# Kernel tuning notes

Hardware: AMD Instinct MI355X
Metric: run time of the kernel (lower is better)

The kernel has to match this reference:

```python
import jax, jax.numpy as jnp
import numpy as np

B, C, M, K, V, D, H, A, L, HF = 2, 128, 4, 4, 64, 1024, 16, 64, 4, 2048
E = M + K
EPS = 1e-5
THETA = 10000.0


def _rmsnorm(x, w):
    return x * jax.lax.rsqrt(jnp.mean(x * x, -1, keepdims=True) + EPS) * w


def _l2norm(x):
    n = jnp.sqrt(jnp.sum(x * x, -1, keepdims=True))
    return x / jnp.maximum(n, EPS)


def _rope(x, cos, sin):
    x1, x2 = jnp.split(x, 2, axis=-1)
    return jnp.concatenate([x1 * cos + x2 * sin, -x1 * sin + x2 * cos], -1)


def _forward(x_input, dec_w1, dec_w2, pos_emb, Wqkv, Wo, Wup, Wdown, attn_norm_w, ffn_norm_w, doc):
    b = x_input.shape[0]
    c = x_input.shape[1] // M
    # decoder_w1 then 'b (c m) (k v) -> b c k (m v)', decoder_w2, pos emb
    x = jnp.einsum('bsd,od->bso', x_input, dec_w1)
    x = x.reshape(b, c, M, K, V).transpose(0, 1, 3, 2, 4).reshape(b, c, K, M * V)
    x = jnp.einsum('bcku,du->bckd', x, dec_w2) + pos_emb
    # decoder_include_original_token: prepend original m tokens per block
    x = jnp.concatenate([x_input.reshape(b, c, M, D), x], axis=2).reshape(b, c * E, D)
    s = c * E
    # mask_mod (decoder_global_original_attn): (causal & kv%e<k & same_doc) | same_block
    idx = jnp.arange(s)
    blk = idx // E
    docs = doc[:, blk]  # [b, s]
    doc_m = docs[:, :, None] == docs[:, None, :]
    causal = blk[:, None] >= blk[None, :]
    kv_ok = (idx % E) < K
    same = blk[:, None] == blk[None, :]
    mask = (causal[None] & kv_ok[None, None, :] & doc_m) | same[None]  # [b, s, s]
    # rotary tables (applied post head-split, dim A)
    inv_freq = (1.0 / THETA) ** (jnp.arange(0, A, 2) / A)
    freqs = jnp.arange(s)[:, None] * inv_freq[None, :]
    cos, sin = jnp.cos(freqs), jnp.sin(freqs)  # [s, A/2]
    scale = 1.0 / jnp.sqrt(jnp.float32(A))
    neg = jnp.float32(-1e30)

    def heads(t):
        return t.reshape(b, s, H, A).transpose(0, 2, 1, 3)

    for li in range(L):
        xn = _rmsnorm(x, attn_norm_w[li])
        qkv = jnp.einsum('bsd,od->bso', xn, Wqkv[li])
        q, k, v = jnp.split(qkv, 3, axis=-1)
        q, k, v = heads(q), heads(k), heads(v)
        q, k = _l2norm(q), _l2norm(k)  # qk_norm
        q, k = _rope(q, cos, sin), _rope(k, cos, sin)
        scores = jnp.einsum('bhqa,bhka->bhqk', q, k) * scale
        scores = jnp.where(mask[:, None], scores, neg)
        probs = jax.nn.softmax(scores, axis=-1)
        attn = jnp.einsum('bhqk,bhka->bhqa', probs, v)
        attn = attn.transpose(0, 2, 1, 3).reshape(b, s, D)
        x1_in = jnp.einsum('bsd,od->bso', attn, Wo[li]) + x
        xf = _rmsnorm(x1_in, ffn_norm_w[li])
        up = jnp.einsum('bsd,od->bso', xf, Wup[li])
        u1, u2 = jnp.split(up, 2, axis=-1)
        x = jnp.einsum('bsh,dh->bsd', jax.nn.silu(u1) * u2, Wdown[li]) + x1_in
    # 'b (c e) d -> (b c) e d' then drop original tokens
    return x.reshape(b * c, E, D)[:, M:]


def setup_inputs() -> dict:
    key = jax.random.key(0)
    ks = jax.random.split(key, 10)
    sc = 0.02
    return {
        'x_input': jax.random.normal(ks[0], (B, C * M, D), jnp.float32),
        'doc': jnp.sort(jax.random.randint(ks[1], (B, C), 0, 4), axis=-1),
        'dec_w1': jax.random.normal(ks[2], (K * V, D), jnp.float32) * sc,
        'dec_w2': jax.random.normal(ks[3], (D, M * V), jnp.float32) * sc,
        'pos_emb': jax.random.normal(ks[4], (1, 1, K, D), jnp.float32) * sc,
        'Wqkv': jax.random.normal(ks[5], (L, 3 * D, D), jnp.float32) * sc,
        'Wo': jax.random.normal(ks[6], (L, D, D), jnp.float32) * sc,
        'Wup': jax.random.normal(ks[7], (L, 2 * HF, D), jnp.float32) * sc,
        'Wdown': jax.random.normal(ks[8], (L, D, HF), jnp.float32) * sc,
        'attn_norm_w': jnp.ones((L, D), jnp.float32),
        'ffn_norm_w': jnp.ones((L, D), jnp.float32),
    }


def reference(x_input, doc, dec_w1, dec_w2, pos_emb, Wqkv, Wo, Wup, Wdown, attn_norm_w, ffn_norm_w):
    return _forward(x_input, dec_w1, dec_w2, pos_emb, Wqkv, Wo, Wup, Wdown, attn_norm_w, ffn_norm_w, doc)
```

## Files before the change

kernel.cpp:

```cpp
#include <hip/hip_runtime.h>
#include <hip/hip_bf16.h>

typedef __bf16 bf16;
typedef __bf16 bf16x8 __attribute__((ext_vector_type(8)));
typedef __bf16 bf16x4 __attribute__((ext_vector_type(4)));
typedef float  f32x4  __attribute__((ext_vector_type(4)));

#define MFMA16(a, b, c) __builtin_amdgcn_mfma_f32_16x16x32_bf16(a, b, c, 0, 0, 0)

template <int EPI, int AF32, int BF32, int TM, int TN, int SK = 1>
__global__ __launch_bounds__(256 * SK) void gemm_bt(
    const void* __restrict__ Av, const void* __restrict__ Bv,
    const float* __restrict__ Res, void* __restrict__ Out,
    int Ntot, int Ktot, int lda)
{
    constexpr int PA = TM / 64, PB = TN / 64;
    constexpr int WN = (TN == 128) ? ((TM == 128) ? 2 : 4) : 2;
    constexpr int WM = 4 / WN;
    constexpr int I = TM / (WM * 16), J = TN / (WN * 16);
    __shared__ __align__(16) bf16 As[2][SK][TM][40];
    __shared__ __align__(16) bf16 Bs[2][SK][TN][40];
    static_assert(SK == 1 || sizeof(As) >= TM * TN * 4, "combine buffer fits in As");
    const int tid  = threadIdx.x;
    const int grp  = (SK > 1) ? (tid >> 8) : 0;
    const int t8   = tid & 255;
    const int wave = t8 >> 6, lane = tid & 63;
    const int quad = lane >> 4, l16 = lane & 15;
    const int wm = wave / WN, wn = wave % WN;
    const int rowW = wm * (TM / WM), colW = wn * (TN / WN);
    const int rowBase = blockIdx.y * TM, colBase = blockIdx.x * TN;

    f32x4 acc[I][J];
    const f32x4 z4 = {0.f, 0.f, 0.f, 0.f};
#pragma unroll
    for (int i = 0; i < I; i++)
#pragma unroll
        for (int j = 0; j < J; j++) acc[i][j] = z4;

    float4 rAf[PA][2]; bf16x8 rAb[PA];
    float4 rBf[PB][2]; bf16x8 rBb[PB];

    auto loadTile = [&](int kt) {
#pragma unroll
        for (int p = 0; p < PA; p++) {
            int ch = p * 256 + t8, r = ch >> 2, c8 = (ch & 3) << 3;
            if (AF32) {
                const float* s = (const float*)Av + (size_t)(rowBase + r) * lda + kt + c8;
                rAf[p][0] = *(const float4*)s; rAf[p][1] = *(const float4*)(s + 4);
            } else {
                rAb[p] = *(const bf16x8*)((const bf16*)Av + (size_t)(rowBase + r) * lda + kt + c8);
            }
        }
#pragma unroll
        for (int p = 0; p < PB; p++) {
            int ch = p * 256 + t8, r = ch >> 2, c8 = (ch & 3) << 3;
            if (BF32) {
                const float* s = (const float*)Bv + (size_t)(colBase + r) * Ktot + kt + c8;
                rBf[p][0] = *(const float4*)s; rBf[p][1] = *(const float4*)(s + 4);
            } else {
                rBb[p] = *(const bf16x8*)((const bf16*)Bv + (size_t)(colBase + r) * Ktot + kt + c8);
            }
        }
    };
    auto storeTile = [&](int buf) {
#pragma unroll
        for (int p = 0; p < PA; p++) {
            int ch = p * 256 + t8, r = ch >> 2, c8 = (ch & 3) << 3;
            bf16x8 t;
            if (AF32) {
                t[0]=(bf16)rAf[p][0].x; t[1]=(bf16)rAf[p][0].y; t[2]=(bf16)rAf[p][0].z; t[3]=(bf16)rAf[p][0].w;
                t[4]=(bf16)rAf[p][1].x; t[5]=(bf16)rAf[p][1].y; t[6]=(bf16)rAf[p][1].z; t[7]=(bf16)rAf[p][1].w;
            } else t = rAb[p];
            *(bf16x8*)&As[buf][grp][r][c8] = t;
        }
#pragma unroll
        for (int p = 0; p < PB; p++) {
            int ch = p * 256 + t8, r = ch >> 2, c8 = (ch & 3) << 3;
            bf16x8 t;
            if (BF32) {
                t[0]=(bf16)rBf[p][0].x; t[1]=(bf16)rBf[p][0].y; t[2]=(bf16)rBf[p][0].z; t[3]=(bf16)rBf[p][0].w;
                t[4]=(bf16)rBf[p][1].x; t[5]=(bf16)rBf[p][1].y; t[6]=(bf16)rBf[p][1].z; t[7]=(bf16)rBf[p][1].w;
            } else t = rBb[p];
            *(bf16x8*)&Bs[buf][grp][r][c8] = t;
        }
    };

    const int Kgrp  = Ktot / SK;
    const int kbase = grp * Kgrp;
    loadTile(kbase);
    storeTile(0);
    __syncthreads();
    const int nk = Kgrp >> 5;
    for (int k = 0; k < nk; k++) {
        const bool more = (k + 1) < nk;
        if (more) loadTile(kbase + ((k + 1) << 5));
        const int buf = k & 1;
        bf16x8 af[I], bfr[J];
#pragma unroll
        for (int i = 0; i < I; i++)
            af[i] = *(const bf16x8*)&As[buf][grp][rowW + i * 16 + l16][quad * 8];
#pragma unroll
        for (int j = 0; j < J; j++)
            bfr[j] = *(const bf16x8*)&Bs[buf][grp][colW + j * 16 + l16][quad * 8];
#pragma unroll
        for (int i = 0; i < I; i++)
#pragma unroll
            for (int j = 0; j < J; j++)
                acc[i][j] = MFMA16(af[i], bfr[j], acc[i][j]);
        if (more) { storeTile(buf ^ 1); __syncthreads(); }
    }

    if (SK == 2) {
        __syncthreads();
        float* red = (float*)&As[0][0][0][0];
        if (grp == 1) {
#pragma unroll
            for (int i = 0; i < I; i++)
#pragma unroll
                for (int j = 0; j < J; j++)
#pragma unroll
                    for (int r = 0; r < 4; r++)
                        red[(rowW + i * 16 + quad * 4 + r) * TN +
                            (colW + j * 16 + l16)] = acc[i][j][r];
        }
        __syncthreads();
        if (grp != 0) return;
#pragma unroll
        for (int i = 0; i < I; i++)
#pragma unroll
            for (int j = 0; j < J; j++)
#pragma unroll
                for (int r = 0; r < 4; r++)
                    acc[i][j][r] += red[(rowW + i * 16 + quad * 4 + r) * TN +
                                        (colW + j * 16 + l16)];
    }

#pragma unroll
    for (int i = 0; i < I; i++) {
        int row0 = rowBase + rowW + i * 16 + quad * 4;
#pragma unroll
        for (int j = 0; j < J; j++) {
            int col = colBase + colW + j * 16 + l16;
#pragma unroll
            for (int r = 0; r < 4; r++) {
                size_t off = (size_t)(row0 + r) * Ntot + col;
                float v = acc[i][j][r];
                if (EPI == 0)      ((bf16*)Out)[off]  = (bf16)v;
                else if (EPI == 1) ((float*)Out)[off] = v + Res[off];
                else               ((float*)Out)[off] = v;
            }
        }
    }
}

__global__ __launch_bounds__(512) void gemm_up_swiglu(
    const bf16* __restrict__ A, const float* __restrict__ B,
    bf16* __restrict__ Out)
{
    __shared__ __align__(16) bf16 Smem[2][2][256][40];
    const int tid  = threadIdx.x;
    const int grp  = tid >> 8, t8 = tid & 255;
    const int wave = t8 >> 6, lane = tid & 63;
    const int quad = lane >> 4, l16 = lane & 15;
    const int wm = wave >> 1, wn = wave & 1;
    const int rowBase = blockIdx.y * 128, cb = blockIdx.x;

    f32x4 acc[4][4];
    const f32x4 z4 = {0.f, 0.f, 0.f, 0.f};
#pragma unroll
    for (int i = 0; i < 4; i++)
#pragma unroll
        for (int j = 0; j < 4; j++) acc[i][j] = z4;

    bf16x8 rA[2]; float4 rB[2][2];
    auto loadTile = [&](int kt) {
#pragma unroll
        for (int p = 0; p < 2; p++) {
            int ch = p * 256 + t8, r = ch >> 2, c8 = (ch & 3) << 3;
            rA[p] = *(const bf16x8*)(A + (size_t)(rowBase + r) * 1024 + kt + c8);
            int brow = (r >> 6) * 2048 + cb * 64 + (r & 63);
            const float* s = B + (size_t)brow * 1024 + kt + c8;
            rB[p][0] = *(const float4*)s; rB[p][1] = *(const float4*)(s + 4);
        }
    };
    auto storeTile = [&](int buf) {
#pragma unroll
        for (int p = 0; p < 2; p++) {
            int ch = p * 256 + t8, r = ch >> 2, c8 = (ch & 3) << 3;
            *(bf16x8*)&Smem[buf][grp][r][c8] = rA[p];
            bf16x8 t;
            t[0]=(bf16)rB[p][0].x; t[1]=(bf16)rB[p][0].y; t[2]=(bf16)rB[p][0].z; t[3]=(bf16)rB[p][0].w;
            t[4]=(bf16)rB[p][1].x; t[5]=(bf16)rB[p][1].y; t[6]=(bf16)rB[p][1].z; t[7]=(bf16)rB[p][1].w;
            *(bf16x8*)&Smem[buf][grp][128 + r][c8] = t;
        }
    };

    const int kbase = grp * 512;
    loadTile(kbase);
    storeTile(0);
    __syncthreads();
    for (int k = 0; k < 16; k++) {
        const bool more = k < 15;
        if (more) loadTile(kbase + ((k + 1) << 5));
        const int buf = k & 1;
        bf16x8 af[4], bfr[4];
#pragma unroll
        for (int i = 0; i < 4; i++)
            af[i] = *(const bf16x8*)&Smem[buf][grp][wm * 64 + i * 16 + l16][quad * 8];
#pragma unroll
        for (int j = 0; j < 4; j++) {
            int brow = (j < 2) ? (wn * 32 + j * 16) : (64 + wn * 32 + (j - 2) * 16);
            bfr[j] = *(const bf16x8*)&Smem[buf][grp][128 + brow + l16][quad * 8];
        }
#pragma unroll
        for (int i = 0; i < 4; i++)
#pragma unroll
            for (int j = 0; j < 4; j++)
                acc[i][j] = MFMA16(af[i], bfr[j], acc[i][j]);
        if (more) { storeTile(buf ^ 1); __syncthreads(); }
    }

    __syncthreads();
    float* red = (float*)&Smem[0][0][0][0];
    if (grp == 1) {
#pragma unroll
        for (int i = 0; i < 4; i++)
#pragma unroll
            for (int j = 0; j < 4; j++) {
                int brow = ((j < 2) ? (wn * 32 + j * 16)
                                    : (64 + wn * 32 + (j - 2) * 16)) + l16;
#pragma unroll
                for (int r = 0; r < 4; r++)
                    red[(wm * 64 + i * 16 + quad * 4 + r) * 128 + brow] = acc[i][j][r];
            }
    }
    __syncthreads();
    if (grp != 0) return;
#pragma unroll
    for (int i = 0; i < 4; i++)
#pragma unroll
        for (int j = 0; j < 4; j++) {
            int brow = ((j < 2) ? (wn * 32 + j * 16)
                                : (64 + wn * 32 + (j - 2) * 16)) + l16;
#pragma unroll
            for (int r = 0; r < 4; r++)
                acc[i][j][r] += red[(wm * 64 + i * 16 + quad * 4 + r) * 128 + brow];
        }

#pragma unroll
    for (int i = 0; i < 4; i++) {
        int row0 = rowBase + wm * 64 + i * 16 + quad * 4;
#pragma unroll
        for (int jj = 0; jj < 2; jj++) {
            int col = cb * 64 + wn * 32 + jj * 16 + l16;
#pragma unroll
            for (int r = 0; r < 4; r++) {
                float u1 = acc[i][jj][r], u2 = acc[i][jj + 2][r];
                float g = u1 / (1.f + __expf(-u1));
                Out[(size_t)(row0 + r) * 2048 + col] = (bf16)(g * u2);
            }
        }
    }
}

__global__ __launch_bounds__(256) void rmsnorm_k(
    const float* __restrict__ X, const float* __restrict__ W,
    bf16* __restrict__ Out)
{
    const int row = blockIdx.x, tid = threadIdx.x;
    const float4 xv = *(const float4*)(X + (size_t)row * 1024 + tid * 4);
    float ss = xv.x * xv.x + xv.y * xv.y + xv.z * xv.z + xv.w * xv.w;
#pragma unroll
    for (int m = 1; m < 64; m <<= 1) ss += __shfl_xor(ss, m);
    __shared__ float red[4];
    if ((tid & 63) == 0) red[tid >> 6] = ss;
    __syncthreads();
    float tot = red[0] + red[1] + red[2] + red[3];
    float sc = rsqrtf(tot * (1.0f / 1024.0f) + 1e-5f);
    const float4 wv = *(const float4*)(W + tid * 4);
    bf16x4 o;
    o[0] = (bf16)(xv.x * sc * wv.x);
    o[1] = (bf16)(xv.y * sc * wv.y);
    o[2] = (bf16)(xv.z * sc * wv.z);
    o[3] = (bf16)(xv.w * sc * wv.w);
    *(bf16x4*)(Out + (size_t)row * 1024 + tid * 4) = o;
}

__global__ __launch_bounds__(256) void ropetab_k(float* __restrict__ tab)
{
    int i = blockIdx.x * 256 + threadIdx.x;
    int s = i >> 5, j = i & 31;
    float f = (float)s * __expf(-(float)j * 0.2878231366242557f);
    tab[i * 2]     = cosf(f);
    tab[i * 2 + 1] = sinf(f);
}

__global__ __launch_bounds__(256) void qkprep_k(
    bf16* __restrict__ qkv, const float* __restrict__ tab)
{
    int wid  = blockIdx.x * 4 + (threadIdx.x >> 6);
    int lane = threadIdx.x & 63;
    int s = wid & 1023, h = (wid >> 10) & 15, b = (wid >> 14) & 1, op = wid >> 15;
    bf16* addr = qkv + ((size_t)(b * 1024 + s)) * 3072 + op * 1024 + h * 64 + lane;
    float v = (float)*addr;
    float ss = v * v;
#pragma unroll
    for (int m = 1; m < 64; m <<= 1) ss += __shfl_xor(ss, m);
    v /= fmaxf(sqrtf(ss), 1e-5f);
    float2 cssn = ((const float2*)tab)[(s << 5) + (lane & 31)];
    float partner = __shfl_xor(v, 32);
    float o = (lane < 32) ? (v * cssn.x + partner * cssn.y)
                          : (v * cssn.x - partner * cssn.y);
    if (op == 0) o *= 0.125f;
    *addr = (bf16)o;
}

__global__ __launch_bounds__(256) void vtrans_k(
    const bf16* __restrict__ qkv, bf16* __restrict__ Vt,
    float* __restrict__ Oacc, float* __restrict__ lacc)
{
    __shared__ __align__(16) bf16 Ls[64][72];
    const int st = blockIdx.x, h = blockIdx.y, b = blockIdx.z;
    const int tid = threadIdx.x;

    int gi = ((b * 16 + h) * 16 + st) * 256 + tid;
    float* Oz = Oacc + (size_t)gi * 16;
    const float4 zf = {0.f, 0.f, 0.f, 0.f};
    *(float4*)Oz = zf; *(float4*)(Oz + 4) = zf;
    *(float4*)(Oz + 8) = zf; *(float4*)(Oz + 12) = zf;
    if (gi < 32768) lacc[gi] = 0.f;

#pragma unroll
    for (int p = 0; p < 2; p++) {
        int s = p * 32 + (tid >> 3), a0 = (tid & 7) << 3;
        *(bf16x8*)&Ls[s][a0] = *(const bf16x8*)(
            qkv + ((size_t)(b * 1024 + st * 64 + s)) * 3072 + 2048 + h * 64 + a0);
    }
    __syncthreads();
#pragma unroll
    for (int p = 0; p < 2; p++) {
        int a = p * 32 + (tid >> 3), s0 = (tid & 7) << 3;
        bf16x8 v;
#pragma unroll
        for (int j = 0; j < 8; j++) v[j] = Ls[s0 + j][a];
        *(bf16x8*)(Vt + (((size_t)((b * 16 + h) * 64 + a)) << 10) + st * 64 + s0) = v;
    }
}

__global__ __launch_bounds__(256) void attn_part(
    const bf16* __restrict__ qkv, const bf16* __restrict__ Vt,
    const int* __restrict__ doc,
    float* __restrict__ Oacc, float* __restrict__ lacc)
{
    const int h = blockIdx.y, b = blockIdx.z;
    const int tid = threadIdx.x, w = tid >> 6, lane = tid & 63;
    const int quad = lane >> 4, l16 = lane & 15;

    __shared__ __align__(16) char smraw[47616];
    bf16 (*Ks)[64][72]  = (bf16(*)[64][72])(smraw);
    bf16 (*Vs)[64][72]  = (bf16(*)[64][72])(smraw + 18432);
    bf16 (*PsT)[64][20] = (bf16(*)[64][20])(smraw + 36864);
    int* docL           = (int*)(smraw + 47104);

    if (tid < 128) docL[tid] = doc[b * 128 + tid];

    int xr = blockIdx.x, p = 0, c = 0;
    for (;;) {
        int ch = (p >> 2) + 1;
        if (xr < ch) { c = xr; break; }
        xr -= ch; p++;
    }
    const int ck0 = c * 4;
    const int T   = p + 1;
    const int ck1 = (ck0 + 4 < T) ? (ck0 + 4) : T;

    const int g = 4 * p + w;
    const bf16* qp = qkv + ((size_t)(b * 1024 + g * 16 + l16)) * 3072 + h * 64 + quad * 8;
    const bf16x8 qf0 = *(const bf16x8*)qp;
    const bf16x8 qf1 = *(const bf16x8*)(qp + 32);
    const bf16* Kbase = qkv + ((size_t)(b * 1024)) * 3072 + 1024 + h * 64;
    const bf16* Vbase = Vt + (((size_t)((b * 16 + h) * 64)) << 10);

    const f32x4 z4 = {0.f, 0.f, 0.f, 0.f};
    f32x4 O[4] = {z4, z4, z4, z4};
    float lp[4] = {0.f, 0.f, 0.f, 0.f};

    __syncthreads();
    int bq[4], dq[4];
#pragma unroll
    for (int r = 0; r < 4; r++) {
        bq[r] = (g * 16 + quad * 4 + r) >> 3;
        dq[r] = docL[bq[r]];
    }

    bf16x8 rK[2], rV[2];
    auto stageRegs = [&](int kt) {
#pragma unroll
        for (int cc = 0; cc < 2; cc++) {
            int ch = cc * 256 + tid, r = ch >> 3, c8 = (ch & 7) << 3;
            rK[cc] = *(const bf16x8*)(Kbase + (size_t)(kt * 64 + r) * 3072 + c8);
            rV[cc] = *(const bf16x8*)(Vbase + ((size_t)r << 10) + kt * 64 + c8);
        }
    };
    auto stageLDS = [&](int buf) {
#pragma unroll
        for (int cc = 0; cc < 2; cc++) {
            int ch = cc * 256 + tid, r = ch >> 3, c8 = (ch & 7) << 3;
            *(bf16x8*)&Ks[buf][r][c8] = rK[cc];
            *(bf16x8*)&Vs[buf][r][c8] = rV[cc];
        }
    };

    stageRegs(ck0);
    stageLDS(0);
    __syncthreads();
    for (int kt = ck0; kt < ck1; kt++) {
        const bool more = (kt + 1) < ck1;
        if (more) stageRegs(kt + 1);
        const int buf = (kt - ck0) & 1;
        const int k0 = kt * 64;
        f32x4 sf[4];
#pragma unroll
        for (int kg = 0; kg < 4; kg++) {
            const bf16x8 k0f = *(const bf16x8*)&Ks[buf][kg * 16 + l16][quad * 8];
            const bf16x8 k1f = *(const bf16x8*)&Ks[buf][kg * 16 + l16][32 + quad * 8];
            sf[kg] = z4;
            sf[kg] = MFMA16(qf0, k0f, sf[kg]);
            sf[kg] = MFMA16(qf1, k1f, sf[kg]);
        }
        float pvv[4][4];
#pragma unroll
        for (int kg = 0; kg < 4; kg++) {
            int kgi = k0 + kg * 16 + l16;
            int bk  = kgi >> 3;
            int dkv = docL[bk];
            bool kbit = (kgi & 7) < 4;
#pragma unroll
            for (int r = 0; r < 4; r++) {
                bool ok = (bq[r] == bk) || ((bq[r] >= bk) && kbit && (dq[r] == dkv));
                float pp = ok ? __expf(sf[kg][r]) : 0.f;
                pvv[kg][r] = pp;
                lp[r] += pp;
            }
        }
#pragma unroll
        for (int kg = 0; kg < 4; kg++) {
            bf16x4 t4;
#pragma unroll
            for (int r = 0; r < 4; r++) t4[r] = (bf16)pvv[kg][r];
            *(bf16x4*)&PsT[w][kg * 16 + l16][quad * 4] = t4;
        }
        bf16x8 pa0, pa1;
#pragma unroll
        for (int j = 0; j < 8; j++) {
            pa0[j] = PsT[w][quad * 8 + j][l16];
            pa1[j] = PsT[w][32 + quad * 8 + j][l16];
        }
#pragma unroll
        for (int t = 0; t < 4; t++) {
            const bf16x8 v0f = *(const bf16x8*)&Vs[buf][t * 16 + l16][quad * 8];
            const bf16x8 v1f = *(const bf16x8*)&Vs[buf][t * 16 + l16][32 + quad * 8];
            O[t] = MFMA16(pa0, v0f, O[t]);
            O[t] = MFMA16(pa1, v1f, O[t]);
        }
        if (more) stageLDS(buf ^ 1);
        __syncthreads();
    }

    float* Osc = (float*)smraw + w * 1024;
#pragma unroll
    for (int t = 0; t < 4; t++)
#pragma unroll
        for (int r = 0; r < 4; r++)
            Osc[(quad * 4 + r) * 64 + t * 16 + l16] = O[t][r];

#pragma unroll
    for (int r = 0; r < 4; r++) {
#pragma unroll
        for (int m = 1; m < 16; m <<= 1) lp[r] += __shfl_xor(lp[r], m);
    }
    const size_t rowb = (size_t)(b * 1024 + g * 16);
    if (l16 < 4) {
        float myl = (l16 == 0) ? lp[0] : (l16 == 1) ? lp[1] : (l16 == 2) ? lp[2] : lp[3];
        atomicAdd(&lacc[(rowb + quad * 4 + l16) * 16 + h], myl);
    }

    float* Obase = Oacc + rowb * 1024 + h * 64;
#pragma unroll
    for (int i = 0; i < 16; i++)
        atomicAdd(&Obase[(size_t)i * 1024 + lane], Osc[i * 64 + lane]);
}

__global__ __launch_bounds__(256) void attn_norm(
    const float* __restrict__ Oacc, const float* __restrict__ lacc,
    bf16* __restrict__ attnb)
{
    int i8 = (blockIdx.x * 256 + threadIdx.x) * 8;
    int row = i8 >> 10, d0 = i8 & 1023;
    float inv = 1.0f / fmaxf(lacc[row * 16 + (d0 >> 6)], 1e-20f);
    const float4 a = *(const float4*)(Oacc + i8);
    const float4 bvv = *(const float4*)(Oacc + i8 + 4);
    bf16x8 o;
    o[0] = (bf16)(a.x * inv); o[1] = (bf16)(a.y * inv);
    o[2] = (bf16)(a.z * inv); o[3] = (bf16)(a.w * inv);
    o[4] = (bf16)(bvv.x * inv); o[5] = (bf16)(bvv.y * inv);
    o[6] = (bf16)(bvv.z * inv); o[7] = (bf16)(bvv.w * inv);
    *(bf16x8*)(attnb + i8) = o;
}

__global__ __launch_bounds__(256) void permute_k(
    const bf16* __restrict__ t1, bf16* __restrict__ t1p)
{
    int idx = blockIdx.x * 256 + threadIdx.x;
    int u = idx & 255, m = u >> 6, v = u & 63;
    int orow = idx >> 8;
    int k = orow & 3, bc = orow >> 2;
    int b = bc >> 7, c = bc & 127;
    t1p[idx] = t1[((size_t)(b * 512 + c * 4 + m)) * 256 + k * 64 + v];
}

__global__ __launch_bounds__(256) void buildx_k(
    const float* __restrict__ x_input, const float* __restrict__ t2,
    const float* __restrict__ pos_emb, float* __restrict__ xres)
{
    int idx = blockIdx.x * 256 + threadIdx.x;
    int d = idx & 1023, row = idx >> 10;
    int b = row >> 10, rr = row & 1023;
    int c = rr >> 3, e = rr & 7;
    float v;
    if (e < 4)
        v = x_input[((size_t)(b * 512 + c * 4 + e)) * 1024 + d];
    else
        v = t2[((size_t)(b * 512 + c * 4 + (e - 4))) * 1024 + d] +
            pos_emb[(e - 4) * 1024 + d];
    xres[idx] = v;
}

__global__ __launch_bounds__(256) void finalout_k(
    const float* __restrict__ xres, float* __restrict__ out)
{
    int idx = blockIdx.x * 256 + threadIdx.x;
    int d = idx & 1023, t = idx >> 10;
    int kk = t & 3, bc = t >> 2;
    int b = bc >> 7, c = bc & 127;
    out[idx] = xres[((size_t)(b * 1024 + c * 8 + 4 + kk)) * 1024 + d];
}

extern "C" void kernel_launch(void* const* d_in, const int* in_sizes, int n_in,
                              void* d_out, int out_size, void* d_ws, size_t ws_size,
                              hipStream_t stream)
{
    const float* x_input = (const float*)d_in[0];
    const int*   doc     = (const int*)d_in[1];
    const float* dec_w1  = (const float*)d_in[2];
    const float* dec_w2  = (const float*)d_in[3];
    const float* pos_emb = (const float*)d_in[4];
    const float* Wqkv    = (const float*)d_in[5];
    const float* Wo      = (const float*)d_in[6];
    const float* Wup     = (const float*)d_in[7];
    const float* Wdown   = (const float*)d_in[8];
    const float* anw     = (const float*)d_in[9];
    const float* fnw     = (const float*)d_in[10];
    float* out = (float*)d_out;

    char* w = (char*)d_ws;
    float* xres  = (float*)(w);
    bf16*  xn1   = (bf16*)(w + (8u << 20));
    bf16*  xn2   = (bf16*)(w + (8u << 20));
    float* Oacc  = (float*)(w + (8u << 20));
    bf16*  t1    = (bf16*)(w + (8u << 20));
    bf16*  t1p   = (bf16*)(w + (8u << 20) + (512u << 10));
    bf16*  qkv   = (bf16*)(w + (16u << 20));
    float* t2    = (float*)(w + (16u << 20));
    float* x1res = (float*)(w + (16u << 20));
    bf16*  attnb = (bf16*)(w + (24u << 20));
    bf16*  hg    = (bf16*)(w + (24u << 20));
    bf16*  Vt    = (bf16*)(w + (28u << 20));
    float* rtab  = out;
    float* lacc  = out + 131072;

    ropetab_k<<<128, 256, 0, stream>>>(rtab);
    gemm_bt<0, 1, 1, 64, 64><<<dim3(4, 16), 256, 0, stream>>>(
        x_input, dec_w1, nullptr, t1, 256, 1024, 1024);
    permute_k<<<1024, 256, 0, stream>>>(t1, t1p);
    gemm_bt<2, 0, 1, 64, 64><<<dim3(16, 16), 256, 0, stream>>>(
        t1p, dec_w2, nullptr, t2, 1024, 256, 256);
    buildx_k<<<8192, 256, 0, stream>>>(x_input, t2, pos_emb, xres);

    for (int li = 0; li < 4; ++li) {
        rmsnorm_k<<<2048, 256, 0, stream>>>(xres, anw + li * 1024, xn1);
        gemm_bt<0, 0, 1, 128, 128><<<dim3(24, 16), 256, 0, stream>>>(
            xn1, Wqkv + (size_t)li * 3072 * 1024, nullptr, qkv, 3072, 1024, 1024);
        qkprep_k<<<16384, 256, 0, stream>>>(qkv, rtab);
        vtrans_k<<<dim3(16, 16, 2), 256, 0, stream>>>(qkv, Vt, Oacc, lacc);
        attn_part<<<dim3(40, 16, 2), 256, 0, stream>>>(qkv, Vt, doc, Oacc, lacc);
        attn_norm<<<1024, 256, 0, stream>>>(Oacc, lacc, attnb);
        gemm_bt<1, 0, 1, 64, 64, 2><<<dim3(16, 32), 512, 0, stream>>>(
            attnb, Wo + (size_t)li * 1024 * 1024, xres, x1res, 1024, 1024, 1024);
        rmsnorm_k<<<2048, 256, 0, stream>>>(x1res, fnw + li * 1024, xn2);
        gemm_up_swiglu<<<dim3(32, 16), 512, 0, stream>>>(
            xn2, Wup + (size_t)li * 4096 * 1024, hg);
        gemm_bt<1, 0, 1, 64, 64, 2><<<dim3(16, 32), 512, 0, stream>>>(
            hg, Wdown + (size_t)li * 1024 * 2048, x1res, xres, 1024, 2048, 2048);
    }

    finalout_k<<<4096, 256, 0, stream>>>(xres, out);
}
```

Baseline: 898.8 us.

## Pre-convert weights to bf16 and stage GEMM tiles via direct global-to-LDS loads

Each layer's fp32 weights are converted to bf16 in separate kernels before use. The QKV and up/SwiGLU GEMMs are rewritten to load tiles straight into shared memory with global_load_lds, dropping the register round-trip, the in-loop fp32-to-bf16 conversion and the split-K reduction in the SwiGLU kernel. Residual adds are now done in place on xres, and the workspace is reorganised to fit the bf16 weight buffers. The extra conversion passes add bandwidth and launches each layer. The unpadded 32-wide LDS rows may also cause bank conflicts.

```diff
diff --git a/kernel.cpp b/kernel.cpp
--- a/kernel.cpp
+++ b/kernel.cpp
@@ -8,10 +8,17 @@
 
 #define MFMA16(a, b, c) __builtin_amdgcn_mfma_f32_16x16x32_bf16(a, b, c, 0, 0, 0)
 
+__device__ __forceinline__ void gload16(const void* g, void* l)
+{
+    __builtin_amdgcn_global_load_lds(
+        (const __attribute__((address_space(1))) unsigned int*)g,
+        (__attribute__((address_space(3))) unsigned int*)l, 16, 0, 0);
+}
+
 template <int EPI, int AF32, int BF32, int TM, int TN, int SK = 1>
 __global__ __launch_bounds__(256 * SK) void gemm_bt(
     const void* __restrict__ Av, const void* __restrict__ Bv,
-    const float* __restrict__ Res, void* __restrict__ Out,
+    const float* Res, void* Out,
     int Ntot, int Ktot, int lda)
 {
     constexpr int PA = TM / 64, PB = TN / 64;
@@ -153,14 +160,90 @@
     }
 }
 
-__global__ __launch_bounds__(512) void gemm_up_swiglu(
-    const bf16* __restrict__ A, const float* __restrict__ B,
+template <int EPI, int TM, int TN>
+__global__ __launch_bounds__(256) void gemm_bt2(
+    const bf16* __restrict__ A, const bf16* __restrict__ B,
+    const float* Res, void* Out,
+    int Ntot, int Ktot, int lda)
+{
+    constexpr int I = TM / 32, J = TN / 32;
+    __shared__ __align__(16) bf16 As[2][TM][32];
+    __shared__ __align__(16) bf16 Bs[2][TN][32];
+    const int tid = threadIdx.x;
+    const int wave = tid >> 6, lane = tid & 63;
+    const int quad = lane >> 4, l16 = lane & 15;
+    const int wm = wave >> 1, wn = wave & 1;
+    const int rowBase = blockIdx.y * TM, colBase = blockIdx.x * TN;
+
+    f32x4 acc[I][J];
+    const f32x4 z4 = {0.f, 0.f, 0.f, 0.f};
+#pragma unroll
+    for (int i = 0; i < I; i++)
+#pragma unroll
+        for (int j = 0; j < J; j++) acc[i][j] = z4;
+
+    auto stage = [&](int kt, int buf) {
+#pragma unroll
+        for (int p = 0; p < TM / 64; p++) {
+            int ch = p * 256 + tid, r = ch >> 2, c8 = (ch & 3) << 3;
+            gload16(A + (size_t)(rowBase + r) * lda + kt + c8,
+                    &As[buf][0][0] + p * 2048 + wave * 512);
+        }
+#pragma unroll
+        for (int p = 0; p < TN / 64; p++) {
+            int ch = p * 256 + tid, r = ch >> 2, c8 = (ch & 3) << 3;
+            gload16(B + (size_t)(colBase + r) * Ktot + kt + c8,
+                    &Bs[buf][0][0] + p * 2048 + wave * 512);
+        }
+    };
+
+    stage(0, 0);
+    __syncthreads();
+    const int nk = Ktot >> 5;
+    for (int k = 0; k < nk; k++) {
+        const int buf = k & 1;
+        if (k + 1 < nk) stage((k + 1) << 5, buf ^ 1);
+        bf16x8 af[I], bfr[J];
+#pragma unroll
+        for (int i = 0; i < I; i++)
+            af[i] = *(const bf16x8*)&As[buf][wm * (TM / 2) + i * 16 + l16][quad * 8];
+#pragma unroll
+        for (int j = 0; j < J; j++)
+            bfr[j] = *(const bf16x8*)&Bs[buf][wn * (TN / 2) + j * 16 + l16][quad * 8];
+#pragma unroll
+        for (int i = 0; i < I; i++)
+#pragma unroll
+            for (int j = 0; j < J; j++)
+                acc[i][j] = MFMA16(af[i], bfr[j], acc[i][j]);
+        __syncthreads();
+    }
+
+#pragma unroll
+    for (int i = 0; i < I; i++) {
+        int row0 = rowBase + wm * (TM / 2) + i * 16 + quad * 4;
+#pragma unroll
+        for (int j = 0; j < J; j++) {
+            int col = colBase + wn * (TN / 2) + j * 16 + l16;
+#pragma unroll
+            for (int r = 0; r < 4; r++) {
+                size_t off = (size_t)(row0 + r) * Ntot + col;
+                float v = acc[i][j][r];
+                if (EPI == 0)      ((bf16*)Out)[off]  = (bf16)v;
+                else if (EPI == 1) ((float*)Out)[off] = v + Res[off];
+                else               ((float*)Out)[off] = v;
+            }
+        }
+    }
+}
+
+__global__ __launch_bounds__(256) void gemm_up_swiglu2(
+    const bf16* __restrict__ A, const bf16* __restrict__ B,
     bf16* __restrict__ Out)
 {
-    __shared__ __align__(16) bf16 Smem[2][2][256][40];
-    const int tid  = threadIdx.x;
-    const int grp  = tid >> 8, t8 = tid & 255;
-    const int wave = t8 >> 6, lane = tid & 63;
+    __shared__ __align__(16) bf16 As[2][128][32];
+    __shared__ __align__(16) bf16 Bs[2][128][32];
+    const int tid = threadIdx.x;
+    const int wave = tid >> 6, lane = tid & 63;
     const int quad = lane >> 4, l16 = lane & 15;
     const int wm = wave >> 1, wn = wave & 1;
     const int rowBase = blockIdx.y * 128, cb = blockIdx.x;
@@ -172,80 +255,39 @@
 #pragma unroll
         for (int j = 0; j < 4; j++) acc[i][j] = z4;
 
-    bf16x8 rA[2]; float4 rB[2][2];
-    auto loadTile = [&](int kt) {
+    auto stage = [&](int kt, int buf) {
 #pragma unroll
         for (int p = 0; p < 2; p++) {
-            int ch = p * 256 + t8, r = ch >> 2, c8 = (ch & 3) << 3;
-            rA[p] = *(const bf16x8*)(A + (size_t)(rowBase + r) * 1024 + kt + c8);
-            int brow = (r >> 6) * 2048 + cb * 64 + (r & 63);
-            const float* s = B + (size_t)brow * 1024 + kt + c8;
-            rB[p][0] = *(const float4*)s; rB[p][1] = *(const float4*)(s + 4);
+            int ch = p * 256 + tid, r = ch >> 2, c8 = (ch & 3) << 3;
+            gload16(A + (size_t)(rowBase + r) * 1024 + kt + c8,
+                    &As[buf][0][0] + p * 2048 + wave * 512);
+            int grow = (r < 64) ? cb * 64 + r : 2048 + cb * 64 + (r - 64);
+            gload16(B + (size_t)grow * 1024 + kt + c8,
+                    &Bs[buf][0][0] + p * 2048 + wave * 512);
         }
     };
-    auto storeTile = [&](int buf) {
-#pragma unroll
-        for (int p = 0; p < 2; p++) {
-            int ch = p * 256 + t8, r = ch >> 2, c8 = (ch & 3) << 3;
-            *(bf16x8*)&Smem[buf][grp][r][c8] = rA[p];
-            bf16x8 t;
-            t[0]=(bf16)rB[p][0].x; t[1]=(bf16)rB[p][0].y; t[2]=(bf16)rB[p][0].z; t[3]=(bf16)rB[p][0].w;
-            t[4]=(bf16)rB[p][1].x; t[5]=(bf16)rB[p][1].y; t[6]=(bf16)rB[p][1].z; t[7]=(bf16)rB[p][1].w;
-            *(bf16x8*)&Smem[buf][grp][128 + r][c8] = t;
-        }
-    };
-
-    const int kbase = grp * 512;
-    loadTile(kbase);
-    storeTile(0);
+
+    stage(0, 0);
     __syncthreads();
-    for (int k = 0; k < 16; k++) {
-        const bool more = k < 15;
-        if (more) loadTile(kbase + ((k + 1) << 5));
+    for (int k = 0; k < 32; k++) {
         const int buf = k & 1;
+        if (k < 31) stage((k + 1) << 5, buf ^ 1);
         bf16x8 af[4], bfr[4];
 #pragma unroll
         for (int i = 0; i < 4; i++)
-            af[i] = *(const bf16x8*)&Smem[buf][grp][wm * 64 + i * 16 + l16][quad * 8];
+            af[i] = *(const bf16x8*)&As[buf][wm * 64 + i * 16 + l16][quad * 8];
 #pragma unroll
         for (int j = 0; j < 4; j++) {
             int brow = (j < 2) ? (wn * 32 + j * 16) : (64 + wn * 32 + (j - 2) * 16);
-            bfr[j] = *(const bf16x8*)&Smem[buf][grp][128 + brow + l16][quad * 8];
+            bfr[j] = *(const bf16x8*)&Bs[buf][brow + l16][quad * 8];
         }
 #pragma unroll
         for (int i = 0; i < 4; i++)
 #pragma unroll
             for (int j = 0; j < 4; j++)
                 acc[i][j] = MFMA16(af[i], bfr[j], acc[i][j]);
-        if (more) { storeTile(buf ^ 1); __syncthreads(); }
-    }
-
-    __syncthreads();
-    float* red = (float*)&Smem[0][0][0][0];
-    if (grp == 1) {
-#pragma unroll
-        for (int i = 0; i < 4; i++)
-#pragma unroll
-            for (int j = 0; j < 4; j++) {
-                int brow = ((j < 2) ? (wn * 32 + j * 16)
-                                    : (64 + wn * 32 + (j - 2) * 16)) + l16;
-#pragma unroll
-                for (int r = 0; r < 4; r++)
-                    red[(wm * 64 + i * 16 + quad * 4 + r) * 128 + brow] = acc[i][j][r];
-            }
-    }
-    __syncthreads();
-    if (grp != 0) return;
-#pragma unroll
-    for (int i = 0; i < 4; i++)
-#pragma unroll
-        for (int j = 0; j < 4; j++) {
-            int brow = ((j < 2) ? (wn * 32 + j * 16)
-                                : (64 + wn * 32 + (j - 2) * 16)) + l16;
-#pragma unroll
-            for (int r = 0; r < 4; r++)
-                acc[i][j][r] += red[(wm * 64 + i * 16 + quad * 4 + r) * 128 + brow];
-        }
+        __syncthreads();
+    }
 
 #pragma unroll
     for (int i = 0; i < 4; i++) {
@@ -261,6 +303,18 @@
             }
         }
     }
+}
+
+__global__ __launch_bounds__(256) void wcvt_k(
+    const float* __restrict__ src, bf16* __restrict__ dst)
+{
+    int i8 = (blockIdx.x * 256 + threadIdx.x) * 8;
+    const float4 a = *(const float4*)(src + i8);
+    const float4 b = *(const float4*)(src + i8 + 4);
+    bf16x8 o;
+    o[0] = (bf16)a.x; o[1] = (bf16)a.y; o[2] = (bf16)a.z; o[3] = (bf16)a.w;
+    o[4] = (bf16)b.x; o[5] = (bf16)b.y; o[6] = (bf16)b.z; o[7] = (bf16)b.w;
+    *(bf16x8*)(dst + i8) = o;
 }
 
 __global__ __launch_bounds__(256) void rmsnorm_k(
@@ -484,7 +538,6 @@
         float myl = (l16 == 0) ? lp[0] : (l16 == 1) ? lp[1] : (l16 == 2) ? lp[2] : lp[3];
         atomicAdd(&lacc[(rowb + quad * 4 + l16) * 16 + h], myl);
     }
-
     float* Obase = Oacc + rowb * 1024 + h * 64;
 #pragma unroll
     for (int i = 0; i < 16; i++)
@@ -564,20 +617,23 @@
     float* out = (float*)d_out;
 
     char* w = (char*)d_ws;
-    float* xres  = (float*)(w);
-    bf16*  xn1   = (bf16*)(w + (8u << 20));
-    bf16*  xn2   = (bf16*)(w + (8u << 20));
-    float* Oacc  = (float*)(w + (8u << 20));
-    bf16*  t1    = (bf16*)(w + (8u << 20));
-    bf16*  t1p   = (bf16*)(w + (8u << 20) + (512u << 10));
-    bf16*  qkv   = (bf16*)(w + (16u << 20));
-    float* t2    = (float*)(w + (16u << 20));
-    float* x1res = (float*)(w + (16u << 20));
-    bf16*  attnb = (bf16*)(w + (24u << 20));
-    bf16*  hg    = (bf16*)(w + (24u << 20));
-    bf16*  Vt    = (bf16*)(w + (28u << 20));
-    float* rtab  = out;
-    float* lacc  = out + 131072;
+    float* xres   = (float*)(w);
+    float* Oacc   = (float*)(w + (8u << 20));
+    bf16*  Wqkv_b = (bf16*)(w + (8u << 20));
+    bf16*  Wup_b  = (bf16*)(w + (8u << 20));
+    bf16*  t1     = (bf16*)(w + (8u << 20));
+    bf16*  t1p    = (bf16*)(w + (8u << 20) + (512u << 10));
+    bf16*  xn1    = (bf16*)(w + (16u << 20));
+    bf16*  Vt     = (bf16*)(w + (16u << 20));
+    bf16*  attnb  = (bf16*)(w + (16u << 20));
+    bf16*  xn2    = (bf16*)(w + (16u << 20));
+    float* t2     = (float*)(w + (16u << 20));
+    bf16*  qkv    = (bf16*)(w + (20u << 20));
+    bf16*  Wo_b   = (bf16*)(w + (20u << 20));
+    bf16*  Wdown_b= (bf16*)(w + (20u << 20));
+    bf16*  hg     = (bf16*)(w + (24u << 20));
+    float* rtab   = out;
+    float* lacc   = out + 131072;
 
     ropetab_k<<<128, 256, 0, stream>>>(rtab);
     gemm_bt<0, 1, 1, 64, 64><<<dim3(4, 16), 256, 0, stream>>>(
@@ -588,20 +644,23 @@
     buildx_k<<<8192, 256, 0, stream>>>(x_input, t2, pos_emb, xres);
 
     for (int li = 0; li < 4; ++li) {
+        wcvt_k<<<1536, 256, 0, stream>>>(Wqkv + (size_t)li * 3072 * 1024, Wqkv_b);
         rmsnorm_k<<<2048, 256, 0, stream>>>(xres, anw + li * 1024, xn1);
-        gemm_bt<0, 0, 1, 128, 128><<<dim3(24, 16), 256, 0, stream>>>(
-            xn1, Wqkv + (size_t)li * 3072 * 1024, nullptr, qkv, 3072, 1024, 1024);
+        gemm_bt2<0, 128, 64><<<dim3(48, 16), 256, 0, stream>>>(
+            xn1, Wqkv_b, nullptr, qkv, 3072, 1024, 1024);
         qkprep_k<<<16384, 256, 0, stream>>>(qkv, rtab);
         vtrans_k<<<dim3(16, 16, 2), 256, 0, stream>>>(qkv, Vt, Oacc, lacc);
         attn_part<<<dim3(40, 16, 2), 256, 0, stream>>>(qkv, Vt, doc, Oacc, lacc);
+        wcvt_k<<<512, 256, 0, stream>>>(Wo + (size_t)li * 1024 * 1024, Wo_b);
         attn_norm<<<1024, 256, 0, stream>>>(Oacc, lacc, attnb);
-        gemm_bt<1, 0, 1, 64, 64, 2><<<dim3(16, 32), 512, 0, stream>>>(
-            attnb, Wo + (size_t)li * 1024 * 1024, xres, x1res, 1024, 1024, 1024);
-        rmsnorm_k<<<2048, 256, 0, stream>>>(x1res, fnw + li * 1024, xn2);
-        gemm_up_swiglu<<<dim3(32, 16), 512, 0, stream>>>(
-            xn2, Wup + (size_t)li * 4096 * 1024, hg);
-        gemm_bt<1, 0, 1, 64, 64, 2><<<dim3(16, 32), 512, 0, stream>>>(
-            hg, Wdown + (size_t)li * 1024 * 2048, x1res, xres, 1024, 2048, 2048);
+        gemm_bt<1, 0, 0, 64, 64, 2><<<dim3(16, 32), 512, 0, stream>>>(
+            attnb, Wo_b, xres, xres, 1024, 1024, 1024);
+        wcvt_k<<<2048, 256, 0, stream>>>(Wup + (size_t)li * 4096 * 1024, Wup_b);
+        wcvt_k<<<1024, 256, 0, stream>>>(Wdown + (size_t)li * 1024 * 2048, Wdown_b);
+        rmsnorm_k<<<2048, 256, 0, stream>>>(xres, fnw + li * 1024, xn2);
+        gemm_up_swiglu2<<<dim3(32, 16), 256, 0, stream>>>(xn2, Wup_b, hg);
+        gemm_bt<1, 0, 0, 64, 64, 2><<<dim3(16, 32), 512, 0, stream>>>(
+            hg, Wdown_b, xres, xres, 1024, 2048, 2048);
     }
 
     finalout_k<<<4096, 256, 0, stream>>>(xres, out);
```

Result: no change. 912.8 us (+1.5%).
